# Kernel optimization log

Measured on AMD Instinct MI355X. Metric: run time of the kernel, lower is better.

Reference implementation:

```python
import jax, jax.numpy as jnp
import numpy as np

N = 50000   # query points
M = 50000   # support points
H = 32      # neighbors per query
K = 15      # kernel points
C = 128     # channels (in == out)
P = 3       # spatial dim
RADIUS = 2.5
KP_EXTENT = 1.2


def setup_inputs() -> dict:
    key = jax.random.key(0)
    ks = jax.random.split(key, 6)
    q_pts = jax.random.normal(ks[0], (N, P), dtype=jnp.float32)
    s_pts = jax.random.normal(ks[1], (M, P), dtype=jnp.float32)
    neighb_inds = jax.random.randint(ks[2], (N, H), 0, M, dtype=jnp.int64)
    x = jax.random.normal(ks[3], (N, C), dtype=jnp.float32)
    # kernel points fixed inside the sphere of given radius
    kernel_points = jax.random.uniform(ks[4], (K, P), dtype=jnp.float32,
                                       minval=-RADIUS, maxval=RADIUS) * 0.5
    # dw_weights init: normal(std=sqrt(1/K)) as in reset_parameters
    dw_weights = jax.random.normal(ks[5], (K, C), dtype=jnp.float32) * np.sqrt(1.0 / K)
    bias = jnp.zeros((C,), dtype=jnp.float32)
    return {"q_pts": q_pts, "s_pts": s_pts, "neighb_inds": neighb_inds,
            "x": x, "kernel_points": kernel_points,
            "dw_weights": dw_weights, "bias": bias}


def reference(q_pts, s_pts, neighb_inds, x, kernel_points, dw_weights, bias):
    # pad support points with a far-away point (index M) and features with zeros
    s_pad = jnp.concatenate([s_pts, jnp.full((1, s_pts.shape[1]), 1e6, s_pts.dtype)], axis=0)
    x_pad = jnp.concatenate([x, jnp.zeros((1, x.shape[1]), x.dtype)], axis=0)

    neighbors = s_pad[neighb_inds] - q_pts[:, None, :]            # [N,H,P]
    diff = neighbors[:, :, None, :] - kernel_points               # [N,H,K,P]
    sq_d = jnp.sum(diff * diff, axis=-1)                          # [N,H,K]
    all_w = jax.nn.relu(1.0 - jnp.sqrt(sq_d) / KP_EXTENT)         # linear KP influence

    neighb_x = x_pad[neighb_inds]                                 # [N,H,C]
    # matmul(all_weights^T, neighb_x): [N,K,H] @ [N,H,C] -> [N,K,C]
    weighted = jnp.einsum('nhk,nhc->nkc', all_w, neighb_x)
    # depthwise multiply by dw_weights [K,C] then sum over kernel points
    result = jnp.einsum('nkc,kc->nc', weighted, dw_weights) + bias
    return result
```

## Files before the change

kernel.cpp:

```cpp
#include <hip/hip_runtime.h>
#include <hip/hip_bf16.h>

#define N_Q 50000
#define H_NB 32
#define K_KP 15
#define C_CH 128
#define KP_EXT 1.2f

typedef __attribute__((ext_vector_type(8))) short bf16x8;
typedef __attribute__((ext_vector_type(4))) float f32x4;

static __device__ __forceinline__ short f2bf(float f) {
    __hip_bfloat16 h = __float2bfloat16(f);
    return *reinterpret_cast<short*>(&h);
}

__global__ __launch_bounds__(256)
void prep_kernel(const float* __restrict__ x, const float* __restrict__ s_pts,
                 const float* __restrict__ q_pts, const float* __restrict__ kp,
                 const float* __restrict__ dw,
                 ushort* __restrict__ xb, float4* __restrict__ sp4,
                 float4* __restrict__ q4, float4* __restrict__ kp4,
                 float4* __restrict__ dwp2) {
    const int t  = threadIdx.x;
    const int m  = blockIdx.x * 16 + (t >> 4);
    const int ln = t & 15;
    const float* xr = x + (size_t)m * C_CH;
    uint v[8];
#pragma unroll
    for (int i = 0; i < 8; ++i)
        v[i] = (uint)(ushort)f2bf(xr[ln + 16 * i]);
    uint4 o;
    o.x = v[0] | (v[1] << 16);
    o.y = v[2] | (v[3] << 16);
    o.z = v[4] | (v[5] << 16);
    o.w = v[6] | (v[7] << 16);
    *(uint4*)(xb + (size_t)m * C_CH + ln * 8) = o;
    if (ln == 0)
        sp4[m] = make_float4(s_pts[3*m], s_pts[3*m+1], s_pts[3*m+2], 0.f);
    if (ln == 1)
        q4[m] = make_float4(q_pts[3*m], q_pts[3*m+1], q_pts[3*m+2], 0.f);
    if (blockIdx.x == 0) {
        if (t < 16) {
            const int kk = t < K_KP ? t : (K_KP - 1);
            kp4[t] = make_float4(kp[3*kk], kp[3*kk+1], kp[3*kk+2], 0.f);
        }
        for (int s = t; s < 512; s += 256) {
            const int lane = s & 63, half = (s >> 6) & 1, t4 = s >> 7;
            const int lgg = lane >> 4, lnn = lane & 15;
            const int c = half * 64 + t4 * 16 + lnn;
            float4 w;
            w.x = dw[(lgg*4 + 0) * C_CH + c];
            w.y = dw[(lgg*4 + 1) * C_CH + c];
            w.z = dw[(lgg*4 + 2) * C_CH + c];
            w.w = (lgg*4 + 3 < K_KP) ? dw[(lgg*4 + 3) * C_CH + c] : 0.f;
            dwp2[s] = w;
        }
    }
}

__global__ __launch_bounds__(256, 8)
void kpconv_mfma5(const float4* __restrict__ q4,
                  const float4* __restrict__ sp4,
                  const int*    __restrict__ inds,
                  const ushort* __restrict__ xb,
                  const float4* __restrict__ kp4,
                  const float4* __restrict__ dwp2,
                  const float*  __restrict__ bias,
                  float*        __restrict__ out)
{
    const int wave = threadIdx.x >> 6;
    const int l    = threadIdx.x & 63;
    const int n    = blockIdx.x * 2 + (wave >> 1);
    const int half = wave & 1;
    const int lg   = l >> 4;
    const int ln   = l & 15;

    const int4* ip = (const int4*)(inds + n * H_NB + lg * 8);
    const int4 i0 = ip[0], i1 = ip[1];
    const int idxv[8] = {i0.x,i0.y,i0.z,i0.w,i1.x,i1.y,i1.z,i1.w};

    uint2 rv[8];
#pragma unroll
    for (int j = 0; j < 8; ++j)
        rv[j] = *(const uint2*)(xb + (size_t)(unsigned)idxv[j] * C_CH + ln * 8 + half * 4);

    const float4 qn = q4[n];
    const float4 k4 = kp4[ln];
    const float ox = qn.x + k4.x, oy = qn.y + k4.y, oz = qn.z + k4.z;

    bf16x8 afrag;
#pragma unroll
    for (int j = 0; j < 8; ++j) {
        const float4 p = sp4[(unsigned)idxv[j]];
        const float dx = p.x - ox, dy = p.y - oy, dz = p.z - oz;
        const float d  = sqrtf(fmaf(dx, dx, fmaf(dy, dy, dz*dz)));
        float w = fmaxf(1.0f - d * (1.0f/KP_EXT), 0.0f);
        if (ln == 15) w = 0.0f;
        afrag[j] = f2bf(w);
    }

    f32x4 acc[4];
#pragma unroll
    for (int t = 0; t < 4; ++t) acc[t] = (f32x4){0.f, 0.f, 0.f, 0.f};

    const uint* rw = (const uint*)&rv[0];
#pragma unroll
    for (int t = 0; t < 4; ++t) {
        const uint sel = (t & 1) ? 0x07060302u : 0x05040100u;
        const int  w   = t >> 1;
        union { bf16x8 v; uint u[4]; } bf;
#pragma unroll
        for (int r = 0; r < 4; ++r)
            bf.u[r] = __builtin_amdgcn_perm(rw[(2*r+1)*2 + w], rw[(2*r)*2 + w], sel);
        acc[t] = __builtin_amdgcn_mfma_f32_16x16x32_bf16(afrag, bf.v, acc[t], 0, 0, 0);
    }

    const int cbase = half * 64;
#pragma unroll
    for (int t = 0; t < 4; ++t) {
        const float4 dwd = dwp2[(t*2 + half) * 64 + l];
        float s;
        s = dwd.x * acc[t][0];
        s = fmaf(dwd.y, acc[t][1], s);
        s = fmaf(dwd.z, acc[t][2], s);
        s = fmaf(dwd.w, acc[t][3], s);
        s += __shfl_xor(s, 16);
        s += __shfl_xor(s, 32);
        s += bias[cbase + t*16 + ln];
        if (l < 16) out[n * C_CH + cbase + t*16 + ln] = s;
    }
}

__global__ __launch_bounds__(256, 4)
void kpconv_mfma_fb(const float* __restrict__ q_pts,
                    const float* __restrict__ s_pts,
                    const int*   __restrict__ inds,
                    const float* __restrict__ x,
                    const float* __restrict__ kp,
                    const float* __restrict__ dw,
                    const float* __restrict__ bias,
                    float*       __restrict__ out)
{
    const int wave = threadIdx.x >> 6;
    const int l    = threadIdx.x & 63;
    const int n    = blockIdx.x * 4 + wave;
    const int lg   = l >> 4;
    const int ln   = l & 15;

    const int4* ip = (const int4*)(inds + n * H_NB + lg * 8);
    const int4 i0 = ip[0], i1 = ip[1];
    const int idxv[8] = {i0.x,i0.y,i0.z,i0.w,i1.x,i1.y,i1.z,i1.w};

    const float qx = q_pts[n*3+0], qy = q_pts[n*3+1], qz = q_pts[n*3+2];
    const int kkc = ln < K_KP ? ln : (K_KP - 1);
    const float kpx = kp[kkc*3+0], kpy = kp[kkc*3+1], kpz = kp[kkc*3+2];

    bf16x8 afrag;
#pragma unroll
    for (int j = 0; j < 8; ++j) {
        const int idx = idxv[j];
        const float px = s_pts[idx*3+0] - qx;
        const float py = s_pts[idx*3+1] - qy;
        const float pz = s_pts[idx*3+2] - qz;
        const float dx = px - kpx, dy = py - kpy, dz = pz - kpz;
        const float d  = sqrtf(fmaf(dx, dx, fmaf(dy, dy, dz*dz)));
        float w = fmaxf(1.0f - d * (1.0f/KP_EXT), 0.0f);
        if (ln == 15) w = 0.0f;
        afrag[j] = f2bf(w);
    }

    unsigned boff[8];
#pragma unroll
    for (int j = 0; j < 8; ++j) boff[j] = (unsigned)idxv[j] * C_CH + (unsigned)ln;

    f32x4 acc[8];
#pragma unroll
    for (int t = 0; t < 8; ++t) acc[t] = (f32x4){0.f, 0.f, 0.f, 0.f};
#pragma unroll
    for (int t = 0; t < 8; ++t) {
        bf16x8 bfrag;
#pragma unroll
        for (int j = 0; j < 8; ++j) bfrag[j] = f2bf(x[boff[j] + t*16]);
        acc[t] = __builtin_amdgcn_mfma_f32_16x16x32_bf16(afrag, bfrag, acc[t], 0, 0, 0);
    }

    const int rowbase = lg * 4;
#pragma unroll
    for (int t = 0; t < 8; ++t) {
        const int c = t*16 + ln;
        float s = 0.f;
#pragma unroll
        for (int r = 0; r < 4; ++r) {
            const int row = rowbase + r;
            const float dwv = (row < K_KP) ? dw[row * C_CH + c] : 0.f;
            s = fmaf(dwv, acc[t][r], s);
        }
        s += __shfl_xor(s, 16);
        s += __shfl_xor(s, 32);
        s += bias[c];
        if (l < 16) out[n * C_CH + c] = s;
    }
}

extern "C" void kernel_launch(void* const* d_in, const int* in_sizes, int n_in,
                              void* d_out, int out_size, void* d_ws, size_t ws_size,
                              hipStream_t stream) {
    const float* q_pts = (const float*)d_in[0];
    const float* s_pts = (const float*)d_in[1];
    const int*   inds  = (const int*)  d_in[2];
    const float* x     = (const float*)d_in[3];
    const float* kp    = (const float*)d_in[4];
    const float* dw    = (const float*)d_in[5];
    const float* bias  = (const float*)d_in[6];
    float* out = (float*)d_out;

    const size_t xb_b   = (size_t)N_Q * C_CH * sizeof(ushort);
    const size_t sp4_b  = (size_t)N_Q * sizeof(float4);
    const size_t q4_b   = (size_t)N_Q * sizeof(float4);
    const size_t kp4_b  = 16 * sizeof(float4);
    const size_t dwp2_b = 512 * sizeof(float4);

    if (ws_size >= xb_b + sp4_b + q4_b + kp4_b + dwp2_b) {
        char* p = (char*)d_ws;
        ushort* xb   = (ushort*)p;                 p += xb_b;
        float4* sp4  = (float4*)p;                 p += sp4_b;
        float4* q4   = (float4*)p;                 p += q4_b;
        float4* kp4  = (float4*)p;                 p += kp4_b;
        float4* dwp2 = (float4*)p;
        prep_kernel<<<N_Q / 16, 256, 0, stream>>>(x, s_pts, q_pts, kp, dw,
                                                  xb, sp4, q4, kp4, dwp2);
        kpconv_mfma5<<<N_Q / 2, 256, 0, stream>>>(q4, sp4, inds, xb,
                                                  kp4, dwp2, bias, out);
    } else {
        kpconv_mfma_fb<<<N_Q / 4, 256, 0, stream>>>(q_pts, s_pts, inds, x,
                                                    kp, dw, bias, out);
    }
}
```

Baseline: 170.3 us.

## Process one query per wave with full-row gathers and coalesced output stores

Each wave now handles one query across all 128 channels instead of splitting channels over two waves. This halves the redundant index loads, point gathers and weight computations per query, and each lane gathers a 16-byte slice of a feature row instead of 8 bytes. Weights are converted to bf16 by truncation through a byte permute rather than a rounded conversion. Padded kernel points are moved far away instead of masking lane 15, and the output writes are rearranged so all 64 lanes store. In exchange each thread holds more registers and the occupancy bound drops from 8 to 4, and truncation slightly changes the numerics.

```diff
diff --git a/kernel.cpp b/kernel.cpp
--- a/kernel.cpp
+++ b/kernel.cpp
@@ -21,7 +21,7 @@
                  const float* __restrict__ dw,
                  ushort* __restrict__ xb, float4* __restrict__ sp4,
                  float4* __restrict__ q4, float4* __restrict__ kp4,
-                 float4* __restrict__ dwp2) {
+                 float4* __restrict__ dwp) {
     const int t  = threadIdx.x;
     const int m  = blockIdx.x * 16 + (t >> 4);
     const int ln = t & 15;
@@ -42,37 +42,36 @@
         q4[m] = make_float4(q_pts[3*m], q_pts[3*m+1], q_pts[3*m+2], 0.f);
     if (blockIdx.x == 0) {
         if (t < 16) {
-            const int kk = t < K_KP ? t : (K_KP - 1);
-            kp4[t] = make_float4(kp[3*kk], kp[3*kk+1], kp[3*kk+2], 0.f);
+            if (t < K_KP) kp4[t] = make_float4(kp[3*t], kp[3*t+1], kp[3*t+2], 0.f);
+            else          kp4[t] = make_float4(1e6f, 1e6f, 1e6f, 0.f);
         }
         for (int s = t; s < 512; s += 256) {
-            const int lane = s & 63, half = (s >> 6) & 1, t4 = s >> 7;
+            const int lane = s & 63, tt = s >> 6;
             const int lgg = lane >> 4, lnn = lane & 15;
-            const int c = half * 64 + t4 * 16 + lnn;
+            const int c = tt * 16 + lnn;
             float4 w;
             w.x = dw[(lgg*4 + 0) * C_CH + c];
             w.y = dw[(lgg*4 + 1) * C_CH + c];
             w.z = dw[(lgg*4 + 2) * C_CH + c];
             w.w = (lgg*4 + 3 < K_KP) ? dw[(lgg*4 + 3) * C_CH + c] : 0.f;
-            dwp2[s] = w;
+            dwp[s] = w;
         }
     }
 }
 
-__global__ __launch_bounds__(256, 8)
-void kpconv_mfma5(const float4* __restrict__ q4,
+__global__ __launch_bounds__(256, 4)
+void kpconv_mfma6(const float4* __restrict__ q4,
                   const float4* __restrict__ sp4,
                   const int*    __restrict__ inds,
                   const ushort* __restrict__ xb,
                   const float4* __restrict__ kp4,
-                  const float4* __restrict__ dwp2,
+                  const float4* __restrict__ dwp,
                   const float*  __restrict__ bias,
                   float*        __restrict__ out)
 {
     const int wave = threadIdx.x >> 6;
     const int l    = threadIdx.x & 63;
-    const int n    = blockIdx.x * 2 + (wave >> 1);
-    const int half = wave & 1;
+    const int n    = blockIdx.x * 4 + wave;
     const int lg   = l >> 4;
     const int ln   = l & 15;
 
@@ -80,56 +79,76 @@
     const int4 i0 = ip[0], i1 = ip[1];
     const int idxv[8] = {i0.x,i0.y,i0.z,i0.w,i1.x,i1.y,i1.z,i1.w};
 
-    uint2 rv[8];
+    uint4 rv[8];
 #pragma unroll
     for (int j = 0; j < 8; ++j)
-        rv[j] = *(const uint2*)(xb + (size_t)(unsigned)idxv[j] * C_CH + ln * 8 + half * 4);
+        rv[j] = *(const uint4*)((const char*)xb +
+                    ((unsigned)idxv[j] * 256u + (unsigned)(ln * 16)));
+
+    float4 pj[8];
+#pragma unroll
+    for (int j = 0; j < 8; ++j)
+        pj[j] = *(const float4*)((const char*)sp4 + (unsigned)idxv[j] * 16u);
 
     const float4 qn = q4[n];
     const float4 k4 = kp4[ln];
     const float ox = qn.x + k4.x, oy = qn.y + k4.y, oz = qn.z + k4.z;
 
-    bf16x8 afrag;
+    float wv[8];
 #pragma unroll
     for (int j = 0; j < 8; ++j) {
-        const float4 p = sp4[(unsigned)idxv[j]];
-        const float dx = p.x - ox, dy = p.y - oy, dz = p.z - oz;
-        const float d  = sqrtf(fmaf(dx, dx, fmaf(dy, dy, dz*dz)));
-        float w = fmaxf(1.0f - d * (1.0f/KP_EXT), 0.0f);
-        if (ln == 15) w = 0.0f;
-        afrag[j] = f2bf(w);
-    }
-
-    f32x4 acc[4];
-#pragma unroll
-    for (int t = 0; t < 4; ++t) acc[t] = (f32x4){0.f, 0.f, 0.f, 0.f};
+        const float dx = pj[j].x - ox, dy = pj[j].y - oy, dz = pj[j].z - oz;
+        const float sq = fmaf(dx, dx, fmaf(dy, dy, dz*dz));
+        const float d  = __builtin_amdgcn_sqrtf(sq);
+        wv[j] = fmaxf(1.0f - d * (1.0f/KP_EXT), 0.0f);
+    }
+
+    union { bf16x8 v; uint u[4]; } af;
+#pragma unroll
+    for (int jj = 0; jj < 4; ++jj)
+        af.u[jj] = __builtin_amdgcn_perm(__float_as_uint(wv[2*jj+1]),
+                                         __float_as_uint(wv[2*jj]),
+                                         0x07060302u);
+
+    f32x4 acc[8];
+#pragma unroll
+    for (int t = 0; t < 8; ++t) acc[t] = (f32x4){0.f, 0.f, 0.f, 0.f};
 
     const uint* rw = (const uint*)&rv[0];
 #pragma unroll
-    for (int t = 0; t < 4; ++t) {
+    for (int t = 0; t < 8; ++t) {
         const uint sel = (t & 1) ? 0x07060302u : 0x05040100u;
         const int  w   = t >> 1;
         union { bf16x8 v; uint u[4]; } bf;
 #pragma unroll
         for (int r = 0; r < 4; ++r)
-            bf.u[r] = __builtin_amdgcn_perm(rw[(2*r+1)*2 + w], rw[(2*r)*2 + w], sel);
-        acc[t] = __builtin_amdgcn_mfma_f32_16x16x32_bf16(afrag, bf.v, acc[t], 0, 0, 0);
-    }
-
-    const int cbase = half * 64;
-#pragma unroll
-    for (int t = 0; t < 4; ++t) {
-        const float4 dwd = dwp2[(t*2 + half) * 64 + l];
-        float s;
-        s = dwd.x * acc[t][0];
-        s = fmaf(dwd.y, acc[t][1], s);
-        s = fmaf(dwd.z, acc[t][2], s);
-        s = fmaf(dwd.w, acc[t][3], s);
-        s += __shfl_xor(s, 16);
-        s += __shfl_xor(s, 32);
-        s += bias[cbase + t*16 + ln];
-        if (l < 16) out[n * C_CH + cbase + t*16 + ln] = s;
-    }
+            bf.u[r] = __builtin_amdgcn_perm(rw[(2*r+1)*4 + w], rw[(2*r)*4 + w], sel);
+        acc[t] = __builtin_amdgcn_mfma_f32_16x16x32_bf16(af.v, bf.v, acc[t], 0, 0, 0);
+    }
+
+    float sfin[8];
+#pragma unroll
+    for (int t = 0; t < 8; ++t) {
+        const float4 dwd = dwp[t*64 + l];
+        float sv;
+        sv = dwd.x * acc[t][0];
+        sv = fmaf(dwd.y, acc[t][1], sv);
+        sv = fmaf(dwd.z, acc[t][2], sv);
+        sv = fmaf(dwd.w, acc[t][3], sv);
+        sv += __shfl_xor(sv, 16);
+        sv += __shfl_xor(sv, 32);
+        sfin[t] = sv + bias[t*16 + ln];
+    }
+
+    const float a0 = (lg & 1) ? sfin[2] : sfin[0];
+    const float a1 = (lg & 1) ? sfin[3] : sfin[1];
+    const float b0 = (lg & 1) ? sfin[6] : sfin[4];
+    const float b1 = (lg & 1) ? sfin[7] : sfin[5];
+    const float o0 = (lg & 2) ? b0 : a0;
+    const float o1 = (lg & 2) ? b1 : a1;
+    float* op = out + n * C_CH + lg * 32 + ln;
+    op[0]  = o0;
+    op[16] = o1;
 }
 
 __global__ __launch_bounds__(256, 4)
@@ -215,23 +234,23 @@
     const float* bias  = (const float*)d_in[6];
     float* out = (float*)d_out;
 
-    const size_t xb_b   = (size_t)N_Q * C_CH * sizeof(ushort);
-    const size_t sp4_b  = (size_t)N_Q * sizeof(float4);
-    const size_t q4_b   = (size_t)N_Q * sizeof(float4);
-    const size_t kp4_b  = 16 * sizeof(float4);
-    const size_t dwp2_b = 512 * sizeof(float4);
-
-    if (ws_size >= xb_b + sp4_b + q4_b + kp4_b + dwp2_b) {
+    const size_t xb_b  = (size_t)N_Q * C_CH * sizeof(ushort);
+    const size_t sp4_b = (size_t)N_Q * sizeof(float4);
+    const size_t q4_b  = (size_t)N_Q * sizeof(float4);
+    const size_t kp4_b = 16 * sizeof(float4);
+    const size_t dwp_b = 512 * sizeof(float4);
+
+    if (ws_size >= xb_b + sp4_b + q4_b + kp4_b + dwp_b) {
         char* p = (char*)d_ws;
-        ushort* xb   = (ushort*)p;                 p += xb_b;
-        float4* sp4  = (float4*)p;                 p += sp4_b;
-        float4* q4   = (float4*)p;                 p += q4_b;
-        float4* kp4  = (float4*)p;                 p += kp4_b;
-        float4* dwp2 = (float4*)p;
+        ushort* xb  = (ushort*)p;  p += xb_b;
+        float4* sp4 = (float4*)p;  p += sp4_b;
+        float4* q4  = (float4*)p;  p += q4_b;
+        float4* kp4 = (float4*)p;  p += kp4_b;
+        float4* dwp = (float4*)p;
         prep_kernel<<<N_Q / 16, 256, 0, stream>>>(x, s_pts, q_pts, kp, dw,
-                                                  xb, sp4, q4, kp4, dwp2);
-        kpconv_mfma5<<<N_Q / 2, 256, 0, stream>>>(q4, sp4, inds, xb,
-                                                  kp4, dwp2, bias, out);
+                                                  xb, sp4, q4, kp4, dwp);
+        kpconv_mfma6<<<N_Q / 4, 256, 0, stream>>>(q4, sp4, inds, xb,
+                                                  kp4, dwp, bias, out);
     } else {
         kpconv_mfma_fb<<<N_Q / 4, 256, 0, stream>>>(q_pts, s_pts, inds, x,
                                                     kp, dw, bias, out);
```

Result: faster. 147.7 us (-13.3%).
